# Optimization experiments

Measured on AMD Instinct MI355X. Metric: run time of the kernel, lower is better.

Reference implementation:

```python
import jax, jax.numpy as jnp
import numpy as np

B, N = 16, 48
NODE, EDGE, HID, MSG, LAYERS, TGT = 32, 16, 64, 64, 3, 128
NL = 128  # hidden width of cfg.net_layers / cfg.layers MLPs


def _lin(key, i, o):
    k1, k2 = jax.random.split(key)
    return (jax.random.normal(k1, (i, o), jnp.float32) * 0.05,
            jax.random.normal(k2, (o,), jnp.float32) * 0.05)


def setup_inputs() -> dict:
    key = jax.random.key(0)
    ks = jax.random.split(key, 16)
    g = (jax.random.uniform(ks[0], (B, N, N)) < 0.5).astype(jnp.float32)
    h0 = jax.random.normal(ks[1], (B, N, NODE), jnp.float32)
    e = jax.random.normal(ks[2], (B, N, N, EDGE), jnp.float32)
    msg_w0, msg_b0 = _lin(ks[3], EDGE, NL)
    msg_w1, msg_b1 = _lin(ks[4], NL, NL)
    msg_w2, msg_b2 = _lin(ks[5], NL, MSG * HID)
    gru_wih = jax.random.normal(ks[6], (3 * HID, MSG), jnp.float32) * 0.05
    gru_whh = jax.random.normal(ks[7], (3 * HID, HID), jnp.float32) * 0.05
    gru_bih = jax.random.normal(ks[8], (3 * HID,), jnp.float32) * 0.05
    gru_bhh = jax.random.normal(ks[9], (3 * HID,), jnp.float32) * 0.05
    r0_w0, r0_b0 = _lin(ks[10], 2 * HID, NL)
    r0_w1, r0_b1 = _lin(ks[11], NL, NL)
    r0_w2, r0_b2 = _lin(ks[12], NL, TGT)
    r1_w0, r1_b0 = _lin(ks[13], HID, NL)
    r1_w1, r1_b1 = _lin(ks[14], NL, NL)
    r1_w2, r1_b2 = _lin(ks[15], NL, TGT)
    return dict(g=g, h0=h0, e=e,
                msg_w0=msg_w0, msg_b0=msg_b0, msg_w1=msg_w1, msg_b1=msg_b1,
                msg_w2=msg_w2, msg_b2=msg_b2,
                gru_wih=gru_wih, gru_whh=gru_whh, gru_bih=gru_bih, gru_bhh=gru_bhh,
                r0_w0=r0_w0, r0_b0=r0_b0, r0_w1=r0_w1, r0_b1=r0_b1, r0_w2=r0_w2, r0_b2=r0_b2,
                r1_w0=r1_w0, r1_b0=r1_b0, r1_w1=r1_w1, r1_b1=r1_b1, r1_w2=r1_w2, r1_b2=r1_b2)


def _net(x, w0, b0, w1, b1, w2, b2):
    # Net: relu hidden layers, linear output (matches torch Net with 2 hidden layers)
    x = jax.nn.relu(x @ w0 + b0)
    x = jax.nn.relu(x @ w1 + b1)
    return x @ w2 + b2


def _gru_step(x, h, wih, whh, bih, bhh):
    # torch.nn.GRU single step; gate order r, z, n
    gi = x @ wih.T + bih
    gh = h @ whh.T + bhh
    r = jax.nn.sigmoid(gi[:, :HID] + gh[:, :HID])
    z = jax.nn.sigmoid(gi[:, HID:2 * HID] + gh[:, HID:2 * HID])
    n = jnp.tanh(gi[:, 2 * HID:] + r * gh[:, 2 * HID:])
    return (1.0 - z) * n + z * h


def reference(g, h0, e,
              msg_w0, msg_b0, msg_w1, msg_b1, msg_w2, msg_b2,
              gru_wih, gru_whh, gru_bih, gru_bhh,
              r0_w0, r0_b0, r0_w1, r0_b1, r0_w2, r0_b2,
              r1_w0, r1_b0, r1_w1, r1_b1, r1_w2, r1_b2):
    # pad h0 up to hidden size
    h_first = jnp.concatenate(
        [h0, jnp.zeros((B, N, HID - NODE), h0.dtype)], axis=2)
    node_mask = (jnp.sum(h0, axis=2) > 0).astype(h0.dtype)[..., None]  # [B,N,1]

    # per-edge weight matrices from edge features (same every layer in the
    # original torch code, so compute once): [B*N*N, MSG, HID]
    m_w = _net(e.reshape(-1, EDGE), msg_w0, msg_b0, msg_w1, msg_b1,
               msg_w2, msg_b2).reshape(-1, MSG, HID)

    h_t = h_first
    for _ in range(LAYERS):
        h_feat = h_t.reshape(-1, HID)  # [B*N, HID]
        # faithful to torch: expand on last dim then view(-1, HID),
        # which interleaves the hidden and neighbor axes in memory order
        h_w_rows = jnp.broadcast_to(
            h_feat[:, :, None], (B * N, HID, N)).reshape(-1, HID)
        msg = jnp.einsum('emh,eh->em', m_w, h_w_rows)  # [B*N*N, MSG]
        msg = msg.reshape(B, N, N, MSG)
        agg = jnp.sum(g[..., None] * msg, axis=1)  # masked sum over dim 1 -> [B,N,MSG]
        h_new = _gru_step(agg.reshape(-1, MSG), h_t.reshape(-1, HID),
                          gru_wih, gru_whh, gru_bih, gru_bhh).reshape(B, N, HID)
        h_t = node_mask * h_new

    # readout: Net0(cat[h_0, h_T]) * Net1(h_T), masked by h_0 activity, summed over nodes
    gate_in = jnp.concatenate([h_first, h_t], axis=-1)  # [B,N,2*HID]
    nn_res = (_net(gate_in, r0_w0, r0_b0, r0_w1, r0_b1, r0_w2, r0_b2) *
              _net(h_t, r1_w0, r1_b0, r1_w1, r1_b1, r1_w2, r1_b2))  # [B,N,TGT]
    read_mask = (jnp.sum(h_first, axis=2) > 0).astype(nn_res.dtype)[..., None]
    res = jnp.sum(read_mask * nn_res, axis=1)  # [B,TGT]
    return jax.nn.sigmoid(res)
```

## Files before the change

### kernel.cpp

```cpp
#include <hip/hip_runtime.h>
#include <cmath>

#define B_ 16
#define N_ 48

__device__ __forceinline__ float sigmoidf_(float x){ return 1.0f/(1.0f+expf(-x)); }

__global__ __launch_bounds__(256) void k_mlp_prep(
    const float* __restrict__ ein, const float* __restrict__ w0, const float* __restrict__ b0,
    const float* __restrict__ w1, const float* __restrict__ b1,
    const float* __restrict__ w2, const float* __restrict__ b2,
    const float* __restrict__ h0,
    const float* __restrict__ wih, const float* __restrict__ whh,
    float* __restrict__ relu2T,
    float* __restrict__ A, float* __restrict__ Bm,
    float* __restrict__ Ab, float* __restrict__ Bb,
    float* __restrict__ hfirst, float* __restrict__ mask,
    float* __restrict__ wihT, float* __restrict__ whhT,
    float* __restrict__ accum, unsigned* __restrict__ cnt)
{
    __shared__ __align__(16) float x1s[32*132];

    if (blockIdx.x >= 1152){
        int idx = (blockIdx.x - 1152)*256 + threadIdx.x;
        if (idx < 24576) {
            int r = idx >> 13;
            int c = (idx >> 6) & 127;
            int m = idx & 63;
            int t = 48 - 16*r;
            const float* src = w2 + c*4096 + m*64;
            float a = 0.f, b = 0.f;
            for (int k = 0; k < 64; k++){ float v = src[k]; if (k < t) a += v; else b += v; }
            A[idx] = a; Bm[idx] = b;
        } else if (idx < 24768) {
            int i2 = idx - 24576;
            int r = i2 >> 6, m = i2 & 63;
            int t = 48 - 16*r;
            const float* src = b2 + m*64;
            float a = 0.f, b = 0.f;
            for (int k = 0; k < 64; k++){ float v = src[k]; if (k < t) a += v; else b += v; }
            Ab[i2] = a; Bb[i2] = b;
        } else if (idx < 73920) {
            int i3 = idx - 24768;
            int node = i3 >> 6, m = i3 & 63;
            hfirst[i3] = (m < 32) ? h0[node*32 + m] : 0.f;
            if (m == 0) {
                float s = 0.f;
                for (int k = 0; k < 32; k++) s += h0[node*32 + k];
                mask[node] = (s > 0.f) ? 1.f : 0.f;
            }
        } else if (idx < 98496) {
            int i4 = idx - 73920;
            if (i4 < 12288) {
                int k = i4 / 192, col = i4 - k*192;
                wihT[i4] = wih[col*64 + k];
            } else {
                int i5 = i4 - 12288;
                int k = i5 / 192, col = i5 - k*192;
                whhT[i5] = whh[col*64 + k];
            }
        } else if (idx < 100544) {
            int i6 = idx - 98496;
            accum[i6] = 0.f;
        } else if (idx < 100560) {
            cnt[idx - 100544] = 0u;
        }
        return;
    }

    int tid = threadIdx.x;
    int et = tid & 15, o0 = (tid >> 4) * 8;
    size_t e0 = (size_t)blockIdx.x * 32;

    float acc[2][8];
    {
        float4 ba = *(const float4*)&b0[o0];
        float4 bb = *(const float4*)&b0[o0 + 4];
        #pragma unroll
        for (int q = 0; q < 2; q++){
            acc[q][0]=ba.x; acc[q][1]=ba.y; acc[q][2]=ba.z; acc[q][3]=ba.w;
            acc[q][4]=bb.x; acc[q][5]=bb.y; acc[q][6]=bb.z; acc[q][7]=bb.w;
        }
    }
    #pragma unroll
    for (int i4 = 0; i4 < 4; i4++){
        float4 ev[2];
        #pragma unroll
        for (int q = 0; q < 2; q++)
            ev[q] = *(const float4*)&ein[(e0 + q*16 + et)*16 + i4*4];
        #pragma unroll
        for (int d = 0; d < 4; d++){
            int i = i4*4 + d;
            float4 wa = *(const float4*)&w0[i*128 + o0];
            float4 wb = *(const float4*)&w0[i*128 + o0 + 4];
            #pragma unroll
            for (int q = 0; q < 2; q++){
                float xi = (d==0) ? ev[q].x : (d==1) ? ev[q].y : (d==2) ? ev[q].z : ev[q].w;
                acc[q][0] += xi*wa.x; acc[q][1] += xi*wa.y;
                acc[q][2] += xi*wa.z; acc[q][3] += xi*wa.w;
                acc[q][4] += xi*wb.x; acc[q][5] += xi*wb.y;
                acc[q][6] += xi*wb.z; acc[q][7] += xi*wb.w;
            }
        }
    }
    #pragma unroll
    for (int q = 0; q < 2; q++){
        int el = q*16 + et;
        *(float4*)&x1s[el*132 + o0] =
            make_float4(fmaxf(acc[q][0],0.f), fmaxf(acc[q][1],0.f),
                        fmaxf(acc[q][2],0.f), fmaxf(acc[q][3],0.f));
        *(float4*)&x1s[el*132 + o0 + 4] =
            make_float4(fmaxf(acc[q][4],0.f), fmaxf(acc[q][5],0.f),
                        fmaxf(acc[q][6],0.f), fmaxf(acc[q][7],0.f));
    }
    __syncthreads();

    float a2[2][8];
    {
        float4 ba = *(const float4*)&b1[o0];
        float4 bb = *(const float4*)&b1[o0 + 4];
        #pragma unroll
        for (int q = 0; q < 2; q++){
            a2[q][0]=ba.x; a2[q][1]=ba.y; a2[q][2]=ba.z; a2[q][3]=ba.w;
            a2[q][4]=bb.x; a2[q][5]=bb.y; a2[q][6]=bb.z; a2[q][7]=bb.w;
        }
    }
    for (int i4 = 0; i4 < 32; i4++){
        int i = i4*4;
        float4 w0a = *(const float4*)&w1[(size_t)(i+0)*128 + o0];
        float4 w0b = *(const float4*)&w1[(size_t)(i+0)*128 + o0 + 4];
        float4 w1a = *(const float4*)&w1[(size_t)(i+1)*128 + o0];
        float4 w1b = *(const float4*)&w1[(size_t)(i+1)*128 + o0 + 4];
        float4 w2a = *(const float4*)&w1[(size_t)(i+2)*128 + o0];
        float4 w2b = *(const float4*)&w1[(size_t)(i+2)*128 + o0 + 4];
        float4 w3a = *(const float4*)&w1[(size_t)(i+3)*128 + o0];
        float4 w3b = *(const float4*)&w1[(size_t)(i+3)*128 + o0 + 4];
        float4 xv[2];
        #pragma unroll
        for (int q = 0; q < 2; q++)
            xv[q] = *(const float4*)&x1s[(q*16 + et)*132 + i];
        #pragma unroll
        for (int q = 0; q < 2; q++){
            float4 x = xv[q];
            a2[q][0] += x.x*w0a.x + x.y*w1a.x + x.z*w2a.x + x.w*w3a.x;
            a2[q][1] += x.x*w0a.y + x.y*w1a.y + x.z*w2a.y + x.w*w3a.y;
            a2[q][2] += x.x*w0a.z + x.y*w1a.z + x.z*w2a.z + x.w*w3a.z;
            a2[q][3] += x.x*w0a.w + x.y*w1a.w + x.z*w2a.w + x.w*w3a.w;
            a2[q][4] += x.x*w0b.x + x.y*w1b.x + x.z*w2b.x + x.w*w3b.x;
            a2[q][5] += x.x*w0b.y + x.y*w1b.y + x.z*w2b.y + x.w*w3b.y;
            a2[q][6] += x.x*w0b.z + x.y*w1b.z + x.z*w2b.z + x.w*w3b.z;
            a2[q][7] += x.x*w0b.w + x.y*w1b.w + x.z*w2b.w + x.w*w3b.w;
        }
    }
    #pragma unroll
    for (int q = 0; q < 2; q++){
        size_t e = e0 + q*16 + et;
        int b  = (int)(e / 2304);
        int rm = (int)(e - (size_t)b*2304);
        int i  = rm / 48;
        int j  = rm - i*48;
        size_t off = (((size_t)(b*48 + j)*48) + i)*128;
        float4 s0 = make_float4(fmaxf(a2[q][0],0.f), fmaxf(a2[q][1],0.f),
                                fmaxf(a2[q][2],0.f), fmaxf(a2[q][3],0.f));
        float4 s1 = make_float4(fmaxf(a2[q][4],0.f), fmaxf(a2[q][5],0.f),
                                fmaxf(a2[q][6],0.f), fmaxf(a2[q][7],0.f));
        *(float4*)&relu2T[off + o0]     = s0;
        *(float4*)&relu2T[off + o0 + 4] = s1;
    }
}

__global__ __launch_bounds__(256) void k_layer(
    const float* __restrict__ hin, float* __restrict__ hout,
    const float* __restrict__ relu2T,
    const float* __restrict__ A, const float* __restrict__ Bm,
    const float* __restrict__ Ab, const float* __restrict__ Bb,
    const float* __restrict__ g, const float* __restrict__ mask,
    const float* __restrict__ wihT, const float* __restrict__ whhT,
    const float* __restrict__ bih, const float* __restrict__ bhh)
{
    int bj = blockIdx.x;
    int b = bj / 48, j = bj - b*48;
    int r = j % 3;
    int p0 = j + j/3;
    int tid = threadIdx.x;
    int base = b*48;
    __shared__ float hs[64], wAs[48], wBs[48];
    __shared__ float pU[2][128], pV[2][128];
    __shared__ float Us[128], Vs[128];
    __shared__ float pC[4][64];
    __shared__ float sAB[2];
    __shared__ float aggs[64], gi[192], gh[192];

    if (tid < 64) hs[tid] = hin[(size_t)bj*64 + tid];
    else if (tid < 112){
        int i = tid - 64;
        int node = base + i;
        float gv = g[(size_t)node*48 + j];
        wAs[i] = gv * hin[(size_t)node*64 + p0];
        wBs[i] = gv * hin[(size_t)node*64 + p0 + 1];
    }
    __syncthreads();
    if (tid < 2){
        const float* src = tid ? wBs : wAs;
        float s = 0.f;
        for (int i = 0; i < 48; i++) s += src[i];
        sAB[tid] = s;
    }
    {
        int c = tid & 127, half = tid >> 7;
        const float* r2b = relu2T + (size_t)bj*6144 + c;
        float aU = 0.f, aV = 0.f;
        for (int ii = 0; ii < 24; ii++){
            int i = half*24 + ii;
            float v = r2b[i*128];
            aU += wAs[i]*v; aV += wBs[i]*v;
        }
        pU[half][c] = aU; pV[half][c] = aV;
    }
    __syncthreads();
    if (tid < 128){ Us[tid] = pU[0][tid] + pU[1][tid]; Vs[tid] = pV[0][tid] + pV[1][tid]; }
    __syncthreads();
    {
        int m = tid & 63, cg = tid >> 6;
        const float* Arp = A  + r*8192 + m;
        const float* Brp = Bm + r*8192 + m;
        float a = 0.f;
        for (int cc = 0; cc < 32; cc++){
            int c = cg*32 + cc;
            a += Us[c]*Arp[c*64] + Vs[c]*Brp[c*64];
        }
        pC[cg][m] = a;
    }
    __syncthreads();
    if (tid < 64){
        aggs[tid] = pC[0][tid] + pC[1][tid] + pC[2][tid] + pC[3][tid]
                  + sAB[0]*Ab[r*64 + tid] + sAB[1]*Bb[r*64 + tid];
    }
    __syncthreads();
    if (tid < 192){
        float gacc = bih[tid], hacc = bhh[tid];
        for (int k = 0; k < 64; k++){
            gacc += aggs[k] * wihT[k*192 + tid];
            hacc += hs[k]   * whhT[k*192 + tid];
        }
        gi[tid] = gacc; gh[tid] = hacc;
    }
    __syncthreads();
    if (tid < 64){
        float rr = sigmoidf_(gi[tid] + gh[tid]);
        float zz = sigmoidf_(gi[64+tid] + gh[64+tid]);
        float nn = tanhf(gi[128+tid] + rr*gh[128+tid]);
        float hnew = (1.f - zz)*nn + zz*hs[tid];
        hout[(size_t)bj*64 + tid] = mask[bj] * hnew;
    }
}

__device__ __forceinline__ void rd_layer(
    const float* __restrict__ Xs, const float* __restrict__ W,
    const float* __restrict__ bias, float* __restrict__ Ys,
    int dim, int o, int ng, bool do_relu)
{
    float a0 = bias[o];
    float a1 = a0;
    for (int i = 0; i < dim; i += 4){
        float w0 = W[(size_t)(i+0)*128 + o];
        float w1 = W[(size_t)(i+1)*128 + o];
        float w2 = W[(size_t)(i+2)*128 + o];
        float w3 = W[(size_t)(i+3)*128 + o];
        const float4 x0 = *(const float4*)&Xs[ng*128 + i];
        const float4 x1 = *(const float4*)&Xs[(ng+2)*128 + i];
        a0 += x0.x*w0 + x0.y*w1 + x0.z*w2 + x0.w*w3;
        a1 += x1.x*w0 + x1.y*w1 + x1.z*w2 + x1.w*w3;
    }
    if (do_relu){ a0 = fmaxf(a0, 0.f); a1 = fmaxf(a1, 0.f); }
    Ys[ng*128 + o] = a0;
    Ys[(ng+2)*128 + o] = a1;
}

__global__ __launch_bounds__(256) void k_read_final(
    const float* __restrict__ hfirst, const float* __restrict__ hT,
    const float* __restrict__ mask,
    const float* __restrict__ w00, const float* __restrict__ b00,
    const float* __restrict__ w01, const float* __restrict__ b01,
    const float* __restrict__ w02, const float* __restrict__ b02,
    const float* __restrict__ w10, const float* __restrict__ b10,
    const float* __restrict__ w11, const float* __restrict__ b11,
    const float* __restrict__ w12, const float* __restrict__ b12,
    float* __restrict__ accum, unsigned* __restrict__ cnt,
    float* __restrict__ out)
{
    __shared__ __align__(16) float xs[4*128];
    __shared__ __align__(16) float ys[4*128];
    __shared__ __align__(16) float zs[4*128];
    __shared__ __align__(16) float os0[4*128];
    __shared__ float mS[4];
    __shared__ unsigned fin;
    int tid = threadIdx.x;
    int b = blockIdx.x / 12, gg = blockIdx.x - b*12;
    int node0 = b*48 + gg*4;
    int o = tid & 127, ng = tid >> 7;
    if (tid < 4) mS[tid] = mask[node0 + tid];
    for (int i = tid; i < 4*128; i += 256){
        int r = i >> 7, c = i & 127;
        xs[i] = (c < 64) ? hfirst[(size_t)(node0+r)*64 + c]
                         : hT[(size_t)(node0+r)*64 + (c - 64)];
    }
    __syncthreads();
    rd_layer(xs,      w00, b00, ys,  128, o, ng, true);  __syncthreads();
    rd_layer(ys,      w01, b01, zs,  128, o, ng, true);  __syncthreads();
    rd_layer(zs,      w02, b02, os0, 128, o, ng, false); __syncthreads();
    rd_layer(xs + 64, w10, b10, ys,  64,  o, ng, true);  __syncthreads();
    rd_layer(ys,      w11, b11, zs,  128, o, ng, true);  __syncthreads();
    {
        float a0 = b12[o];
        float a1 = a0;
        for (int i = 0; i < 128; i += 4){
            float w0 = w12[(size_t)(i+0)*128 + o];
            float w1 = w12[(size_t)(i+1)*128 + o];
            float w2 = w12[(size_t)(i+2)*128 + o];
            float w3 = w12[(size_t)(i+3)*128 + o];
            const float4 x0 = *(const float4*)&zs[ng*128 + i];
            const float4 x1 = *(const float4*)&zs[(ng+2)*128 + i];
            a0 += x0.x*w0 + x0.y*w1 + x0.z*w2 + x0.w*w3;
            a1 += x1.x*w0 + x1.y*w1 + x1.z*w2 + x1.w*w3;
        }
        float s = mS[ng]   * os0[ng*128 + o]     * a0
                + mS[ng+2] * os0[(ng+2)*128 + o] * a1;
        __syncthreads();
        ys[ng*128 + o] = s;
    }
    __syncthreads();
    if (tid < 128)
        atomicAdd(&accum[(size_t)b*128 + tid], ys[tid] + ys[128 + tid]);
    __syncthreads();
    if (tid == 0){
        __threadfence();
        fin = atomicAdd(&cnt[b], 1u);
    }
    __syncthreads();
    if (fin == 11u && tid < 128){
        float v = atomicAdd(&accum[(size_t)b*128 + tid], 0.f);
        out[(size_t)b*128 + tid] = 1.0f / (1.0f + expf(-v));
    }
}

extern "C" void kernel_launch(void* const* d_in, const int* in_sizes, int n_in,
                              void* d_out, int out_size, void* d_ws, size_t ws_size,
                              hipStream_t stream)
{
    (void)in_sizes; (void)n_in; (void)out_size; (void)ws_size;
    const float* g    = (const float*)d_in[0];
    const float* h0   = (const float*)d_in[1];
    const float* e    = (const float*)d_in[2];
    const float* mw0  = (const float*)d_in[3];
    const float* mb0  = (const float*)d_in[4];
    const float* mw1  = (const float*)d_in[5];
    const float* mb1  = (const float*)d_in[6];
    const float* mw2  = (const float*)d_in[7];
    const float* mb2  = (const float*)d_in[8];
    const float* wih  = (const float*)d_in[9];
    const float* whh  = (const float*)d_in[10];
    const float* bih  = (const float*)d_in[11];
    const float* bhh  = (const float*)d_in[12];
    const float* r0w0 = (const float*)d_in[13];
    const float* r0b0 = (const float*)d_in[14];
    const float* r0w1 = (const float*)d_in[15];
    const float* r0b1 = (const float*)d_in[16];
    const float* r0w2 = (const float*)d_in[17];
    const float* r0b2 = (const float*)d_in[18];
    const float* r1w0 = (const float*)d_in[19];
    const float* r1b0 = (const float*)d_in[20];
    const float* r1w1 = (const float*)d_in[21];
    const float* r1b1 = (const float*)d_in[22];
    const float* r1w2 = (const float*)d_in[23];
    const float* r1b2 = (const float*)d_in[24];
    float* out = (float*)d_out;

    float* ws     = (float*)d_ws;
    float* A      = ws;
    float* Bm     = A      + 24576;
    float* Ab     = Bm     + 24576;
    float* Bb     = Ab     + 192;
    float* hfirst = Bb     + 192;
    float* hA     = hfirst + 49152;
    float* hB     = hA     + 49152;
    float* mask   = hB     + 49152;
    float* wihT   = mask   + 768;
    float* whhT   = wihT   + 12288;
    float* accum  = whhT   + 12288;
    unsigned* cnt = (unsigned*)(accum + 2048);
    float* relu2T = accum  + 2048 + 64;

    k_mlp_prep<<<1545, 256, 0, stream>>>(e, mw0, mb0, mw1, mb1, mw2, mb2, h0,
                                         wih, whh, relu2T,
                                         A, Bm, Ab, Bb, hfirst, mask,
                                         wihT, whhT, accum, cnt);
    k_layer<<<768, 256, 0, stream>>>(hfirst, hA, relu2T, A, Bm, Ab, Bb, g, mask,
                                     wihT, whhT, bih, bhh);
    k_layer<<<768, 256, 0, stream>>>(hA, hB, relu2T, A, Bm, Ab, Bb, g, mask,
                                     wihT, whhT, bih, bhh);
    k_layer<<<768, 256, 0, stream>>>(hB, hA, relu2T, A, Bm, Ab, Bb, g, mask,
                                     wihT, whhT, bih, bhh);
    k_read_final<<<192, 256, 0, stream>>>(hfirst, hA, mask,
                                          r0w0, r0b0, r0w1, r0b1, r0w2, r0b2,
                                          r1w0, r1b0, r1w1, r1b1, r1w2, r1b2,
                                          accum, cnt, out);
}
```

Baseline: 223.0 us.

## Store edge MLP activations in natural order and double edges per block

The edge MLP prep kernel now handles 64 edges per block instead of 32, which halves the number of compute blocks and reuses each loaded weight vector across twice as many edges. It also writes the second hidden layer in natural edge order rather than a transposed layout, which removes the index division and gives contiguous stores. The layer kernel now reads those activations with a 6144-float stride per source node instead of contiguous rows, so its reads are less coalesced across rows. Register pressure and shared memory per block in the prep kernel also grow.

```diff
diff --git a/kernel.cpp b/kernel.cpp
--- a/kernel.cpp
+++ b/kernel.cpp
@@ -12,17 +12,17 @@
     const float* __restrict__ w2, const float* __restrict__ b2,
     const float* __restrict__ h0,
     const float* __restrict__ wih, const float* __restrict__ whh,
-    float* __restrict__ relu2T,
+    float* __restrict__ relu2,
     float* __restrict__ A, float* __restrict__ Bm,
     float* __restrict__ Ab, float* __restrict__ Bb,
     float* __restrict__ hfirst, float* __restrict__ mask,
     float* __restrict__ wihT, float* __restrict__ whhT,
     float* __restrict__ accum, unsigned* __restrict__ cnt)
 {
-    __shared__ __align__(16) float x1s[32*132];
-
-    if (blockIdx.x >= 1152){
-        int idx = (blockIdx.x - 1152)*256 + threadIdx.x;
+    __shared__ __align__(16) float x1s[64*132];
+
+    if (blockIdx.x >= 576){
+        int idx = (blockIdx.x - 576)*256 + threadIdx.x;
         if (idx < 24576) {
             int r = idx >> 13;
             int c = (idx >> 6) & 127;
@@ -60,8 +60,7 @@
                 whhT[i5] = whh[col*64 + k];
             }
         } else if (idx < 100544) {
-            int i6 = idx - 98496;
-            accum[i6] = 0.f;
+            accum[idx - 98496] = 0.f;
         } else if (idx < 100560) {
             cnt[idx - 100544] = 0u;
         }
@@ -70,23 +69,23 @@
 
     int tid = threadIdx.x;
     int et = tid & 15, o0 = (tid >> 4) * 8;
-    size_t e0 = (size_t)blockIdx.x * 32;
-
-    float acc[2][8];
+    size_t e0 = (size_t)blockIdx.x * 64;
+
+    float acc[4][8];
     {
         float4 ba = *(const float4*)&b0[o0];
         float4 bb = *(const float4*)&b0[o0 + 4];
         #pragma unroll
-        for (int q = 0; q < 2; q++){
+        for (int q = 0; q < 4; q++){
             acc[q][0]=ba.x; acc[q][1]=ba.y; acc[q][2]=ba.z; acc[q][3]=ba.w;
             acc[q][4]=bb.x; acc[q][5]=bb.y; acc[q][6]=bb.z; acc[q][7]=bb.w;
         }
     }
     #pragma unroll
     for (int i4 = 0; i4 < 4; i4++){
-        float4 ev[2];
-        #pragma unroll
-        for (int q = 0; q < 2; q++)
+        float4 ev[4];
+        #pragma unroll
+        for (int q = 0; q < 4; q++)
             ev[q] = *(const float4*)&ein[(e0 + q*16 + et)*16 + i4*4];
         #pragma unroll
         for (int d = 0; d < 4; d++){
@@ -94,7 +93,7 @@
             float4 wa = *(const float4*)&w0[i*128 + o0];
             float4 wb = *(const float4*)&w0[i*128 + o0 + 4];
             #pragma unroll
-            for (int q = 0; q < 2; q++){
+            for (int q = 0; q < 4; q++){
                 float xi = (d==0) ? ev[q].x : (d==1) ? ev[q].y : (d==2) ? ev[q].z : ev[q].w;
                 acc[q][0] += xi*wa.x; acc[q][1] += xi*wa.y;
                 acc[q][2] += xi*wa.z; acc[q][3] += xi*wa.w;
@@ -104,7 +103,7 @@
         }
     }
     #pragma unroll
-    for (int q = 0; q < 2; q++){
+    for (int q = 0; q < 4; q++){
         int el = q*16 + et;
         *(float4*)&x1s[el*132 + o0] =
             make_float4(fmaxf(acc[q][0],0.f), fmaxf(acc[q][1],0.f),
@@ -115,12 +114,12 @@
     }
     __syncthreads();
 
-    float a2[2][8];
+    float a2[4][8];
     {
         float4 ba = *(const float4*)&b1[o0];
         float4 bb = *(const float4*)&b1[o0 + 4];
         #pragma unroll
-        for (int q = 0; q < 2; q++){
+        for (int q = 0; q < 4; q++){
             a2[q][0]=ba.x; a2[q][1]=ba.y; a2[q][2]=ba.z; a2[q][3]=ba.w;
             a2[q][4]=bb.x; a2[q][5]=bb.y; a2[q][6]=bb.z; a2[q][7]=bb.w;
         }
@@ -135,12 +134,12 @@
         float4 w2b = *(const float4*)&w1[(size_t)(i+2)*128 + o0 + 4];
         float4 w3a = *(const float4*)&w1[(size_t)(i+3)*128 + o0];
         float4 w3b = *(const float4*)&w1[(size_t)(i+3)*128 + o0 + 4];
-        float4 xv[2];
-        #pragma unroll
-        for (int q = 0; q < 2; q++)
+        float4 xv[4];
+        #pragma unroll
+        for (int q = 0; q < 4; q++)
             xv[q] = *(const float4*)&x1s[(q*16 + et)*132 + i];
         #pragma unroll
-        for (int q = 0; q < 2; q++){
+        for (int q = 0; q < 4; q++){
             float4 x = xv[q];
             a2[q][0] += x.x*w0a.x + x.y*w1a.x + x.z*w2a.x + x.w*w3a.x;
             a2[q][1] += x.x*w0a.y + x.y*w1a.y + x.z*w2a.y + x.w*w3a.y;
@@ -153,25 +152,20 @@
         }
     }
     #pragma unroll
-    for (int q = 0; q < 2; q++){
+    for (int q = 0; q < 4; q++){
         size_t e = e0 + q*16 + et;
-        int b  = (int)(e / 2304);
-        int rm = (int)(e - (size_t)b*2304);
-        int i  = rm / 48;
-        int j  = rm - i*48;
-        size_t off = (((size_t)(b*48 + j)*48) + i)*128;
         float4 s0 = make_float4(fmaxf(a2[q][0],0.f), fmaxf(a2[q][1],0.f),
                                 fmaxf(a2[q][2],0.f), fmaxf(a2[q][3],0.f));
         float4 s1 = make_float4(fmaxf(a2[q][4],0.f), fmaxf(a2[q][5],0.f),
                                 fmaxf(a2[q][6],0.f), fmaxf(a2[q][7],0.f));
-        *(float4*)&relu2T[off + o0]     = s0;
-        *(float4*)&relu2T[off + o0 + 4] = s1;
+        *(float4*)&relu2[e*128 + o0]     = s0;
+        *(float4*)&relu2[e*128 + o0 + 4] = s1;
     }
 }
 
 __global__ __launch_bounds__(256) void k_layer(
     const float* __restrict__ hin, float* __restrict__ hout,
-    const float* __restrict__ relu2T,
+    const float* __restrict__ relu2,
     const float* __restrict__ A, const float* __restrict__ Bm,
     const float* __restrict__ Ab, const float* __restrict__ Bb,
     const float* __restrict__ g, const float* __restrict__ mask,
@@ -208,11 +202,11 @@
     }
     {
         int c = tid & 127, half = tid >> 7;
-        const float* r2b = relu2T + (size_t)bj*6144 + c;
+        const float* r2b = relu2 + ((size_t)base*48 + j)*128 + c;
         float aU = 0.f, aV = 0.f;
         for (int ii = 0; ii < 24; ii++){
             int i = half*24 + ii;
-            float v = r2b[i*128];
+            float v = r2b[(size_t)i*6144];
             aU += wAs[i]*v; aV += wBs[i]*v;
         }
         pU[half][c] = aU; pV[half][c] = aV;
@@ -389,17 +383,17 @@
     float* whhT   = wihT   + 12288;
     float* accum  = whhT   + 12288;
     unsigned* cnt = (unsigned*)(accum + 2048);
-    float* relu2T = accum  + 2048 + 64;
-
-    k_mlp_prep<<<1545, 256, 0, stream>>>(e, mw0, mb0, mw1, mb1, mw2, mb2, h0,
-                                         wih, whh, relu2T,
-                                         A, Bm, Ab, Bb, hfirst, mask,
-                                         wihT, whhT, accum, cnt);
-    k_layer<<<768, 256, 0, stream>>>(hfirst, hA, relu2T, A, Bm, Ab, Bb, g, mask,
+    float* relu2  = accum  + 2048 + 64;
+
+    k_mlp_prep<<<969, 256, 0, stream>>>(e, mw0, mb0, mw1, mb1, mw2, mb2, h0,
+                                        wih, whh, relu2,
+                                        A, Bm, Ab, Bb, hfirst, mask,
+                                        wihT, whhT, accum, cnt);
+    k_layer<<<768, 256, 0, stream>>>(hfirst, hA, relu2, A, Bm, Ab, Bb, g, mask,
                                      wihT, whhT, bih, bhh);
-    k_layer<<<768, 256, 0, stream>>>(hA, hB, relu2T, A, Bm, Ab, Bb, g, mask,
+    k_layer<<<768, 256, 0, stream>>>(hA, hB, relu2, A, Bm, Ab, Bb, g, mask,
                                      wihT, whhT, bih, bhh);
-    k_layer<<<768, 256, 0, stream>>>(hB, hA, relu2T, A, Bm, Ab, Bb, g, mask,
+    k_layer<<<768, 256, 0, stream>>>(hB, hA, relu2, A, Bm, Ab, Bb, g, mask,
                                      wihT, whhT, bih, bhh);
     k_read_final<<<192, 256, 0, stream>>>(hfirst, hA, mask,
                                           r0w0, r0b0, r0w1, r0b1, r0w2, r0b2,
```

Measured after the change: 192.8 us. 1.16x faster.
